# Kernel tuning notes

Measured on AMD Instinct MI355X. Metric: run time of the kernel, lower is better.

Reference implementation:

```python
import jax, jax.numpy as jnp
import numpy as np

ALPHA = 0.2          # LeakyReLU negative slope
NEG_BIG = -9e15      # mask fill value from the original code
N, IN_F, OUT_F = 8192, 128, 64


def setup_inputs() -> dict:
    key = jax.random.key(0)
    k1, k2, k3, k4 = jax.random.split(key, 4)
    h = jax.random.normal(k1, (N, IN_F), dtype=jnp.float32)
    adj = jax.random.randint(k2, (N, N), 0, 2, dtype=jnp.int32)
    W = jax.random.normal(k3, (IN_F, OUT_F), dtype=jnp.float32) * 0.1
    a = jax.random.normal(k4, (2 * OUT_F, 1), dtype=jnp.float32) * 0.1
    return {"h": h, "adj": adj, "W": W, "a": a}


def reference(h, adj, W, a):
    # Wh: [N, F]
    Wh = h @ W
    # e_ij = leakyrelu([Wh_i ; Wh_j] . a) = leakyrelu(Wh_i.a1 + Wh_j.a2)
    # (identical math to the original NxNx2F concat, without materializing it)
    a1 = a[:OUT_F, 0]   # [F]
    a2 = a[OUT_F:, 0]   # [F]
    s1 = Wh @ a1        # [N]
    s2 = Wh @ a2        # [N]
    e = jax.nn.leaky_relu(s1[:, None] + s2[None, :], negative_slope=ALPHA)  # [N, N]
    e = jnp.where(adj > 0, e, jnp.float32(NEG_BIG))
    attention = jax.nn.softmax(e, axis=1)
    # dropout is identity at inference (training=False)
    h_prime = attention @ Wh  # [N, F]
    return jax.nn.elu(h_prime)  # concat=True -> elu
```

## Files before the change

### kernel.cpp

```cpp
#include <hip/hip_runtime.h>
#include <hip/hip_bf16.h>

#define N 8192
#define IN_F 128
#define OUT_F 64
#define LRELU_ALPHA 0.2f
#define NEG_BIG -9000000000000000.0f
#define NCHUNK 4

typedef __attribute__((ext_vector_type(8))) short short8;
typedef __attribute__((ext_vector_type(4))) float float4v;

__device__ __forceinline__ unsigned short bf16_bits(float x) {
  unsigned u = __builtin_bit_cast(unsigned, x);
  u += 0x7fffu + ((u >> 16) & 1u);
  return (unsigned short)(u >> 16);
}

__global__ __launch_bounds__(256) void prep_kernel(
    const float* __restrict__ h, const float* __restrict__ W,
    const float* __restrict__ a, float* __restrict__ s1,
    float* __restrict__ s2, unsigned short* __restrict__ whT) {
  const int tid = threadIdx.x;
  const int row = blockIdx.x * 4 + (tid >> 6);
  const int k = tid & 63;
  const float* hr = h + row * IN_F;
  float acc = 0.f;
#pragma unroll 8
  for (int c = 0; c < IN_F; ++c) acc = fmaf(hr[c], W[c * OUT_F + k], acc);
  whT[(long)k * N + row] = bf16_bits(acc);
  float p1 = acc * a[k];
  float p2 = acc * a[OUT_F + k];
#pragma unroll
  for (int off = 32; off > 0; off >>= 1) {
    p1 += __shfl_xor(p1, off);
    p2 += __shfl_xor(p2, off);
  }
  if (k == 0) { s1[row] = p1; s2[row] = p2; }
}

__global__ __launch_bounds__(256) void gat_partial_kernel(
    const int* __restrict__ adj, const float* __restrict__ s1,
    const float* __restrict__ s2, const unsigned short* __restrict__ whT,
    float* __restrict__ pacc, float* __restrict__ pl) {
  __shared__ float lds_acc[4][16][65];
  __shared__ float lds_l[4][16];

  const int tid = threadIdx.x;
  const int wave = tid >> 6;
  const int lane = tid & 63;
  const int r16 = lane & 15;
  const int quad = lane >> 4;
  const int row0 = blockIdx.x * 16;
  const int chunk = blockIdx.y;
  const int col0 = chunk * 2048 + wave * 512;

  const float s1r = s1[row0 + r16];
  const long adj_base = (long)(row0 + r16) * N;

  float lsum = 0.f;
  float4v acc0 = {0.f, 0.f, 0.f, 0.f};
  float4v acc1 = {0.f, 0.f, 0.f, 0.f};
  float4v acc2 = {0.f, 0.f, 0.f, 0.f};
  float4v acc3 = {0.f, 0.f, 0.f, 0.f};

  for (int t = 0; t < 16; ++t) {
    const int j0 = col0 + t * 32 + quad * 8;
    const int4* ap = (const int4*)(adj + adj_base + j0);
    const int4 a0 = ap[0];
    const int4 a1 = ap[1];
    const float4* sp = (const float4*)(s2 + j0);
    const float4 s20 = sp[0], s21 = sp[1];
    const unsigned short* bp = whT + (long)r16 * N + j0;
    const short8 b0 = *(const short8*)(bp + 0L * 16 * N);
    const short8 b1 = *(const short8*)(bp + 1L * 16 * N);
    const short8 b2 = *(const short8*)(bp + 2L * 16 * N);
    const short8 b3 = *(const short8*)(bp + 3L * 16 * N);

    float se[8] = {s20.x, s20.y, s20.z, s20.w, s21.x, s21.y, s21.z, s21.w};
    int am[8] = {a0.x, a0.y, a0.z, a0.w, a1.x, a1.y, a1.z, a1.w};
    short8 afrag;
#pragma unroll
    for (int i = 0; i < 8; ++i) {
      float tv = s1r + se[i];
      tv = fmaxf(tv, LRELU_ALPHA * tv);
      const float e = am[i] > 0 ? tv : NEG_BIG;
      const float p = __expf(e);
      lsum += p;
      afrag[i] = (short)bf16_bits(p);
    }
    acc0 = __builtin_amdgcn_mfma_f32_16x16x32_bf16(afrag, b0, acc0, 0, 0, 0);
    acc1 = __builtin_amdgcn_mfma_f32_16x16x32_bf16(afrag, b1, acc1, 0, 0, 0);
    acc2 = __builtin_amdgcn_mfma_f32_16x16x32_bf16(afrag, b2, acc2, 0, 0, 0);
    acc3 = __builtin_amdgcn_mfma_f32_16x16x32_bf16(afrag, b3, acc3, 0, 0, 0);
  }

  lsum += __shfl_xor(lsum, 16);
  lsum += __shfl_xor(lsum, 32);
  if (lane < 16) lds_l[wave][lane] = lsum;
#pragma unroll
  for (int reg = 0; reg < 4; ++reg) {
    const int r = quad * 4 + reg;
    lds_acc[wave][r][0 * 16 + r16] = acc0[reg];
    lds_acc[wave][r][1 * 16 + r16] = acc1[reg];
    lds_acc[wave][r][2 * 16 + r16] = acc2[reg];
    lds_acc[wave][r][3 * 16 + r16] = acc3[reg];
  }
  __syncthreads();

  {
    const int r = tid >> 4;
    const int k0 = (tid & 15) * 4;
    float v0 = 0.f, v1 = 0.f, v2 = 0.f, v3 = 0.f;
#pragma unroll
    for (int w = 0; w < 4; ++w) {
      v0 += lds_acc[w][r][k0 + 0];
      v1 += lds_acc[w][r][k0 + 1];
      v2 += lds_acc[w][r][k0 + 2];
      v3 += lds_acc[w][r][k0 + 3];
    }
    float4 o = {v0, v1, v2, v3};
    *(float4*)(pacc + ((long)chunk * N + row0 + r) * OUT_F + k0) = o;
    if (tid < 16) {
      float L = lds_l[0][tid] + lds_l[1][tid] + lds_l[2][tid] + lds_l[3][tid];
      pl[(long)chunk * N + row0 + tid] = L;
    }
  }
}

__global__ __launch_bounds__(256) void merge_kernel(
    const float* __restrict__ pacc, const float* __restrict__ pl,
    float* __restrict__ out) {
  const int idx = blockIdx.x * 256 + threadIdx.x;
  const int r = idx >> 4;
  const int k0 = (idx & 15) * 4;
  float4 S = {0.f, 0.f, 0.f, 0.f};
  float L = 0.f;
#pragma unroll
  for (int c = 0; c < NCHUNK; ++c) {
    const float4 p = *(const float4*)(pacc + ((long)c * N + r) * OUT_F + k0);
    S.x += p.x; S.y += p.y; S.z += p.z; S.w += p.w;
    L += pl[(long)c * N + r];
  }
  const float inv = 1.f / L;
  float v[4] = {S.x * inv, S.y * inv, S.z * inv, S.w * inv};
  float4 o;
  o.x = v[0] > 0.f ? v[0] : expm1f(v[0]);
  o.y = v[1] > 0.f ? v[1] : expm1f(v[1]);
  o.z = v[2] > 0.f ? v[2] : expm1f(v[2]);
  o.w = v[3] > 0.f ? v[3] : expm1f(v[3]);
  *(float4*)(out + (long)r * OUT_F + k0) = o;
}

extern "C" void kernel_launch(void* const* d_in, const int* in_sizes, int n_in,
                              void* d_out, int out_size, void* d_ws, size_t ws_size,
                              hipStream_t stream) {
  const float* h = (const float*)d_in[0];
  const int* adj = (const int*)d_in[1];
  const float* W = (const float*)d_in[2];
  const float* a = (const float*)d_in[3];
  float* out = (float*)d_out;

  float* s1 = (float*)d_ws;
  float* s2 = s1 + N;
  unsigned short* whT = (unsigned short*)(s2 + N);
  float* pacc = (float*)(whT + (long)OUT_F * N);
  float* pl = pacc + (long)NCHUNK * N * OUT_F;

  prep_kernel<<<N / 4, 256, 0, stream>>>(h, W, a, s1, s2, whT);
  gat_partial_kernel<<<dim3(N / 16, NCHUNK), 256, 0, stream>>>(adj, s1, s2, whT, pacc, pl);
  merge_kernel<<<N * OUT_F / 1024, 256, 0, stream>>>(pacc, pl, out);
}
```

Before: 444.1 us.

## Fuse column-chunk partials and merge into single 512-thread GAT kernel

The four column-chunk blocks per row tile are replaced by one 512-thread block whose eight waves each cover 1024 columns. Partial sums and softmax denominators are reduced in LDS, and the normalization plus ELU is applied in-kernel. This removes the separate merge launch and the global round trip of the partial accumulators. In exchange the grid shrinks from 2048 blocks to 512, which may reduce occupancy and latency hiding on the adjacency stream.

```diff
diff --git a/kernel.cpp b/kernel.cpp
--- a/kernel.cpp
+++ b/kernel.cpp
@@ -6,7 +6,6 @@
 #define OUT_F 64
 #define LRELU_ALPHA 0.2f
 #define NEG_BIG -9000000000000000.0f
-#define NCHUNK 4
 
 typedef __attribute__((ext_vector_type(8))) short short8;
 typedef __attribute__((ext_vector_type(4))) float float4v;
@@ -39,12 +38,12 @@
   if (k == 0) { s1[row] = p1; s2[row] = p2; }
 }
 
-__global__ __launch_bounds__(256) void gat_partial_kernel(
+__global__ __launch_bounds__(512) void gat_kernel(
     const int* __restrict__ adj, const float* __restrict__ s1,
     const float* __restrict__ s2, const unsigned short* __restrict__ whT,
-    float* __restrict__ pacc, float* __restrict__ pl) {
-  __shared__ float lds_acc[4][16][65];
-  __shared__ float lds_l[4][16];
+    float* __restrict__ out) {
+  __shared__ float lds_acc[8][16][65];
+  __shared__ float lds_l[8][16];
 
   const int tid = threadIdx.x;
   const int wave = tid >> 6;
@@ -52,8 +51,7 @@
   const int r16 = lane & 15;
   const int quad = lane >> 4;
   const int row0 = blockIdx.x * 16;
-  const int chunk = blockIdx.y;
-  const int col0 = chunk * 2048 + wave * 512;
+  const int col0 = wave * 1024;
 
   const float s1r = s1[row0 + r16];
   const long adj_base = (long)(row0 + r16) * N;
@@ -64,7 +62,7 @@
   float4v acc2 = {0.f, 0.f, 0.f, 0.f};
   float4v acc3 = {0.f, 0.f, 0.f, 0.f};
 
-  for (int t = 0; t < 16; ++t) {
+  for (int t = 0; t < 32; ++t) {
     const int j0 = col0 + t * 32 + quad * 8;
     const int4* ap = (const int4*)(adj + adj_base + j0);
     const int4 a0 = ap[0];
@@ -108,48 +106,18 @@
   }
   __syncthreads();
 
-  {
-    const int r = tid >> 4;
-    const int k0 = (tid & 15) * 4;
-    float v0 = 0.f, v1 = 0.f, v2 = 0.f, v3 = 0.f;
 #pragma unroll
-    for (int w = 0; w < 4; ++w) {
-      v0 += lds_acc[w][r][k0 + 0];
-      v1 += lds_acc[w][r][k0 + 1];
-      v2 += lds_acc[w][r][k0 + 2];
-      v3 += lds_acc[w][r][k0 + 3];
+  for (int o = tid; o < 16 * 64; o += 512) {
+    const int r = o >> 6, k = o & 63;
+    float S = 0.f, L = 0.f;
+#pragma unroll
+    for (int w = 0; w < 8; ++w) {
+      S += lds_acc[w][r][k];
+      L += lds_l[w][r];
     }
-    float4 o = {v0, v1, v2, v3};
-    *(float4*)(pacc + ((long)chunk * N + row0 + r) * OUT_F + k0) = o;
-    if (tid < 16) {
-      float L = lds_l[0][tid] + lds_l[1][tid] + lds_l[2][tid] + lds_l[3][tid];
-      pl[(long)chunk * N + row0 + tid] = L;
-    }
+    const float v = S / L;
+    out[(long)(row0 + r) * OUT_F + k] = v > 0.f ? v : expm1f(v);
   }
-}
-
-__global__ __launch_bounds__(256) void merge_kernel(
-    const float* __restrict__ pacc, const float* __restrict__ pl,
-    float* __restrict__ out) {
-  const int idx = blockIdx.x * 256 + threadIdx.x;
-  const int r = idx >> 4;
-  const int k0 = (idx & 15) * 4;
-  float4 S = {0.f, 0.f, 0.f, 0.f};
-  float L = 0.f;
-#pragma unroll
-  for (int c = 0; c < NCHUNK; ++c) {
-    const float4 p = *(const float4*)(pacc + ((long)c * N + r) * OUT_F + k0);
-    S.x += p.x; S.y += p.y; S.z += p.z; S.w += p.w;
-    L += pl[(long)c * N + r];
-  }
-  const float inv = 1.f / L;
-  float v[4] = {S.x * inv, S.y * inv, S.z * inv, S.w * inv};
-  float4 o;
-  o.x = v[0] > 0.f ? v[0] : expm1f(v[0]);
-  o.y = v[1] > 0.f ? v[1] : expm1f(v[1]);
-  o.z = v[2] > 0.f ? v[2] : expm1f(v[2]);
-  o.w = v[3] > 0.f ? v[3] : expm1f(v[3]);
-  *(float4*)(out + (long)r * OUT_F + k0) = o;
 }
 
 extern "C" void kernel_launch(void* const* d_in, const int* in_sizes, int n_in,
@@ -164,10 +132,7 @@
   float* s1 = (float*)d_ws;
   float* s2 = s1 + N;
   unsigned short* whT = (unsigned short*)(s2 + N);
-  float* pacc = (float*)(whT + (long)OUT_F * N);
-  float* pl = pacc + (long)NCHUNK * N * OUT_F;
 
   prep_kernel<<<N / 4, 256, 0, stream>>>(h, W, a, s1, s2, whT);
-  gat_partial_kernel<<<dim3(N / 16, NCHUNK), 256, 0, stream>>>(adj, s1, s2, whT, pacc, pl);
-  merge_kernel<<<N * OUT_F / 1024, 256, 0, stream>>>(pacc, pl, out);
+  gat_kernel<<<N / 16, 512, 0, stream>>>(adj, s1, s2, whT, out);
 }
```

Result: no change. 447.8 us (+0.8%).
